# Kernel tuning notes

Measured on AMD Instinct MI355X. Metric: run time of the kernel, lower is better.

Reference implementation:

```python
import jax, jax.numpy as jnp
import numpy as np

N = 100000
E = 1600000
IN, HID, OUT = 128, 128, 64


def sage_conv(x, edge_index, W_l, W_r, b):
    # PyG SAGEConv with mean aggregation:
    # out = mean_{j in N(i)} x_j @ W_l + x_i @ W_r + b
    src, dst = edge_index[0], edge_index[1]
    msgs = x[src]                                            # [E, D] gather
    summed = jax.ops.segment_sum(msgs, dst, num_segments=N)  # [N, D] scatter-add
    deg = jax.ops.segment_sum(jnp.ones((E,), x.dtype), dst, num_segments=N)
    mean = summed / jnp.maximum(deg, 1.0)[:, None]
    return mean @ W_l + x @ W_r + b


def setup_inputs() -> dict:
    key = jax.random.key(0)
    ks = jax.random.split(key, 8)
    x = jax.random.normal(ks[0], (N, IN), dtype=jnp.float32)
    edge_index = jax.random.randint(ks[1], (2, E), 0, N, dtype=jnp.int64)
    s1 = 1.0 / np.sqrt(IN)
    s2 = 1.0 / np.sqrt(HID)
    W1_l = jax.random.uniform(ks[2], (IN, HID), jnp.float32, -s1, s1)
    W1_r = jax.random.uniform(ks[3], (IN, HID), jnp.float32, -s1, s1)
    b1 = jnp.zeros((HID,), jnp.float32)
    W2_l = jax.random.uniform(ks[4], (HID, OUT), jnp.float32, -s2, s2)
    W2_r = jax.random.uniform(ks[5], (HID, OUT), jnp.float32, -s2, s2)
    b2 = jnp.zeros((OUT,), jnp.float32)
    return {"x": x, "edge_index": edge_index, "W1_l": W1_l, "W1_r": W1_r,
            "b1": b1, "W2_l": W2_l, "W2_r": W2_r, "b2": b2}


def reference(x, edge_index, W1_l, W1_r, b1, W2_l, W2_r, b2):
    h = sage_conv(x, edge_index, W1_l, W1_r, b1)
    h = jax.nn.relu(h)
    out = sage_conv(h, edge_index, W2_l, W2_r, b2)
    return out
```

## Files before the change

### kernel.cpp

```cpp
#include <hip/hip_runtime.h>

#define NN 100000
#define NE 1600000
#define KB 782
#define BSH 7
#define MAXB 4096
#define PBLK 200

#define OFF_CC    0
#define OFF_RST   1024
#define OFF_RDG   101120
#define OFF_STAGE 201216
#define OFF_XB    3404288
#define OFF_XF8   9810432
#define OFF_MEANB 13013504
#define OFF_HB    19419648
#define OFF_W1LP  25825792
#define OFF_W1RP  (25825792 + 8192)
#define OFF_W2LP  (25825792 + 16384)
#define OFF_W2RP  (25825792 + 20480)

typedef __bf16 bf16x8 __attribute__((ext_vector_type(8)));
typedef float f32x4 __attribute__((ext_vector_type(4)));
typedef float f32x2 __attribute__((ext_vector_type(2)));

static __device__ __forceinline__ ushort f2bf(float f) {
    unsigned u = __float_as_uint(f);
    return (ushort)((u + 0x7fffu + ((u >> 16) & 1u)) >> 16);
}
static __device__ __forceinline__ float bflo(unsigned u) { return __uint_as_float(u << 16); }
static __device__ __forceinline__ float bfhi(unsigned u) { return __uint_as_float(u & 0xffff0000u); }

__global__ void cvt_kernel(const float* __restrict__ x, ushort* __restrict__ xb,
                           unsigned* __restrict__ xf8) {
    int i = blockIdx.x * 256 + threadIdx.x;
    float4 v = ((const float4*)x)[i];
    uint2 o;
    o.x = (unsigned)f2bf(v.x) | ((unsigned)f2bf(v.y) << 16);
    o.y = (unsigned)f2bf(v.z) | ((unsigned)f2bf(v.w) << 16);
    ((uint2*)xb)[i] = o;
    int p8 = __builtin_amdgcn_cvt_pk_fp8_f32(v.x, v.y, 0, false);
    p8 = __builtin_amdgcn_cvt_pk_fp8_f32(v.z, v.w, p8, true);
    xf8[i] = (unsigned)p8;
}

__global__ void pack_kernel(const float* __restrict__ W1l, const float* __restrict__ W1r,
                            const float* __restrict__ W2l, const float* __restrict__ W2r,
                            ushort* __restrict__ w1lp, ushort* __restrict__ w1rp,
                            ushort* __restrict__ w2lp, ushort* __restrict__ w2rp) {
    int blk = blockIdx.x;
    const float* W;
    ushort* out;
    int N, frag0;
    if (blk < 8)       { W = W1l; out = w1lp; N = 128; frag0 = blk * 4; }
    else if (blk < 16) { W = W1r; out = w1rp; N = 128; frag0 = (blk - 8) * 4; }
    else if (blk < 20) { W = W2l; out = w2lp; N = 64;  frag0 = (blk - 16) * 4; }
    else               { W = W2r; out = w2rp; N = 64;  frag0 = (blk - 20) * 4; }
    int lane = threadIdx.x & 63;
    int frag = frag0 + (threadIdx.x >> 6);
    int NT = N >> 4;
    int ktile = frag / NT, ntile = frag - ktile * NT;
    int k = ktile * 32 + (lane >> 4) * 8;
    int n = ntile * 16 + (lane & 15);
    ushort tmp[8];
#pragma unroll
    for (int j = 0; j < 8; ++j) tmp[j] = f2bf(W[(k + j) * N + n]);
    uint4 o;
    o.x = (unsigned)tmp[0] | ((unsigned)tmp[1] << 16);
    o.y = (unsigned)tmp[2] | ((unsigned)tmp[3] << 16);
    o.z = (unsigned)tmp[4] | ((unsigned)tmp[5] << 16);
    o.w = (unsigned)tmp[6] | ((unsigned)tmp[7] << 16);
    *(uint4*)&out[(frag * 64 + lane) * 8] = o;
}

__global__ __launch_bounds__(1024) void cpart_kernel(const int* __restrict__ src,
                                                     const int* __restrict__ dst,
                                                     int* __restrict__ cc,
                                                     unsigned* __restrict__ stage) {
    __shared__ int hist[KB];
    __shared__ int cur[KB];
    int t = threadIdx.x;
    int e0 = blockIdx.x * (NE / PBLK);
    int e1 = e0 + (NE / PBLK);
    for (int i = t; i < KB; i += 1024) hist[i] = 0;
    __syncthreads();
    for (int e = e0 + t; e < e1; e += 1024)
        atomicAdd(&hist[dst[e] >> BSH], 1);
    __syncthreads();
    for (int i = t; i < KB; i += 1024) {
        int c = hist[i];
        cur[i] = c ? atomicAdd(&cc[i], c) : 0;
    }
    __syncthreads();
    for (int e = e0 + t; e < e1; e += 1024) {
        int d = dst[e];
        int bkt = d >> BSH;
        int p = atomicAdd(&cur[bkt], 1);
        if (p < MAXB)
            stage[bkt * MAXB + p] = ((unsigned)(d & 127) << 17) | (unsigned)src[e];
    }
}

__global__ __launch_bounds__(256) void sort_kernel(unsigned* __restrict__ stage,
                                                   const int* __restrict__ cc,
                                                   int* __restrict__ rstart,
                                                   int* __restrict__ rdeg) {
    __shared__ unsigned ssrc[MAXB];
    __shared__ int sc[128];
    __shared__ int loff[129];
    __shared__ int lcur[128];
    int t = threadIdx.x;
    int b = blockIdx.x;
    unsigned* st = stage + b * MAXB;
    int cnt = min(cc[b], MAXB);

    if (t < 128) lcur[t] = 0;
    __syncthreads();
    for (int i = t; i < cnt; i += 256) atomicAdd(&lcur[st[i] >> 17], 1);
    __syncthreads();
    if (t < 128) sc[t] = lcur[t];
    __syncthreads();
    for (int off = 1; off < 128; off <<= 1) {
        int v = (t < 128 && t >= off) ? sc[t - off] : 0;
        __syncthreads();
        if (t < 128) sc[t] += v;
        __syncthreads();
    }
    if (t < 128) {
        int excl = (t == 0) ? 0 : sc[t - 1];
        loff[t] = excl;
        lcur[t] = excl;
    }
    if (t == 127) loff[128] = sc[127];
    __syncthreads();
    for (int i = t; i < cnt; i += 256) {
        unsigned v = st[i];
        int p = atomicAdd(&lcur[v >> 17], 1);
        ssrc[p] = v & 0x1FFFFu;
    }
    __syncthreads();
    for (int i = t; i < cnt; i += 256) st[i] = ssrc[i];
    int node0 = b << BSH;
    if (t < 128 && node0 + t < NN) {
        rstart[node0 + t] = b * MAXB + loff[t];
        rdeg[node0 + t] = loff[t + 1] - loff[t];
    }
}

static __device__ __forceinline__ void accum8(float* a, uint2 u) {
    f32x2 p0 = __builtin_amdgcn_cvt_pk_f32_fp8(u.x, false);
    f32x2 p1 = __builtin_amdgcn_cvt_pk_f32_fp8(u.x, true);
    f32x2 p2 = __builtin_amdgcn_cvt_pk_f32_fp8(u.y, false);
    f32x2 p3 = __builtin_amdgcn_cvt_pk_f32_fp8(u.y, true);
    a[0] += p0.x; a[1] += p0.y; a[2] += p1.x; a[3] += p1.y;
    a[4] += p2.x; a[5] += p2.y; a[6] += p3.x; a[7] += p3.y;
}

static __device__ __forceinline__ void writeRow8(ushort* __restrict__ meanb, int node,
                                                 int l4, const float* a, int deg) {
    float inv = 1.0f / fmaxf((float)deg, 1.0f);
    uint4 o;
    o.x = (unsigned)f2bf(a[0] * inv) | ((unsigned)f2bf(a[1] * inv) << 16);
    o.y = (unsigned)f2bf(a[2] * inv) | ((unsigned)f2bf(a[3] * inv) << 16);
    o.z = (unsigned)f2bf(a[4] * inv) | ((unsigned)f2bf(a[5] * inv) << 16);
    o.w = (unsigned)f2bf(a[6] * inv) | ((unsigned)f2bf(a[7] * inv) << 16);
    *(uint4*)&meanb[node * 128 + 8 * l4] = o;
}

__global__ __launch_bounds__(256) void agg1g_kernel(const unsigned* __restrict__ es,
                                                    const int* __restrict__ rstart,
                                                    const int* __restrict__ rdeg,
                                                    const unsigned* __restrict__ xf8,
                                                    ushort* __restrict__ meanb) {
    int t = threadIdx.x;
    int l4 = t & 15;
    int nA = blockIdx.x * 32 + (t >> 4) * 2;
    int nB = nA + 1;
    int sA = rstart[nA], dA = rdeg[nA];
    int sB = rstart[nB], dB = rdeg[nB];
    const uint2* xv = (const uint2*)xf8;
    float aA[8] = {0.f, 0.f, 0.f, 0.f, 0.f, 0.f, 0.f, 0.f};
    float aB[8] = {0.f, 0.f, 0.f, 0.f, 0.f, 0.f, 0.f, 0.f};
    int eA = 0, eB = 0;
    while (eA + 4 <= dA && eB + 4 <= dB) {
        int qa0 = es[sA + eA + 0], qa1 = es[sA + eA + 1];
        int qa2 = es[sA + eA + 2], qa3 = es[sA + eA + 3];
        int qb0 = es[sB + eB + 0], qb1 = es[sB + eB + 1];
        int qb2 = es[sB + eB + 2], qb3 = es[sB + eB + 3];
        uint2 ua0 = xv[qa0 * 16 + l4], ua1 = xv[qa1 * 16 + l4];
        uint2 ua2 = xv[qa2 * 16 + l4], ua3 = xv[qa3 * 16 + l4];
        uint2 ub0 = xv[qb0 * 16 + l4], ub1 = xv[qb1 * 16 + l4];
        uint2 ub2 = xv[qb2 * 16 + l4], ub3 = xv[qb3 * 16 + l4];
        accum8(aA, ua0); accum8(aA, ua1); accum8(aA, ua2); accum8(aA, ua3);
        accum8(aB, ub0); accum8(aB, ub1); accum8(aB, ub2); accum8(aB, ub3);
        eA += 4; eB += 4;
    }
    for (; eA + 4 <= dA; eA += 4) {
        int q0 = es[sA + eA + 0], q1 = es[sA + eA + 1];
        int q2 = es[sA + eA + 2], q3 = es[sA + eA + 3];
        uint2 u0 = xv[q0 * 16 + l4], u1 = xv[q1 * 16 + l4];
        uint2 u2 = xv[q2 * 16 + l4], u3 = xv[q3 * 16 + l4];
        accum8(aA, u0); accum8(aA, u1); accum8(aA, u2); accum8(aA, u3);
    }
    for (; eA < dA; ++eA) accum8(aA, xv[es[sA + eA] * 16 + l4]);
    for (; eB + 4 <= dB; eB += 4) {
        int q0 = es[sB + eB + 0], q1 = es[sB + eB + 1];
        int q2 = es[sB + eB + 2], q3 = es[sB + eB + 3];
        uint2 u0 = xv[q0 * 16 + l4], u1 = xv[q1 * 16 + l4];
        uint2 u2 = xv[q2 * 16 + l4], u3 = xv[q3 * 16 + l4];
        accum8(aB, u0); accum8(aB, u1); accum8(aB, u2); accum8(aB, u3);
    }
    for (; eB < dB; ++eB) accum8(aB, xv[es[sB + eB] * 16 + l4]);

    writeRow8(meanb, nA, l4, aA, dA);
    writeRow8(meanb, nB, l4, aB, dB);
}

__global__ __launch_bounds__(256) void agg2g_kernel(const unsigned* __restrict__ es,
                                                    const int* __restrict__ rstart,
                                                    const int* __restrict__ rdeg,
                                                    const ushort* __restrict__ pb,
                                                    float* __restrict__ meanp) {
    int t = threadIdx.x;
    int l5 = t & 31;
    int nA = blockIdx.x * 16 + (t >> 5) * 2;
    int nB = nA + 1;
    int sA = rstart[nA], dA = rdeg[nA];
    int sB = rstart[nB], dB = rdeg[nB];
    const unsigned* pbu = (const unsigned*)pb;
    float a0 = 0.f, a1 = 0.f, b0 = 0.f, b1 = 0.f;
    int eA = 0, eB = 0;
    while (eA + 4 <= dA && eB + 4 <= dB) {
        int qa0 = es[sA + eA + 0], qa1 = es[sA + eA + 1];
        int qa2 = es[sA + eA + 2], qa3 = es[sA + eA + 3];
        int qb0 = es[sB + eB + 0], qb1 = es[sB + eB + 1];
        int qb2 = es[sB + eB + 2], qb3 = es[sB + eB + 3];
        unsigned ua0 = pbu[qa0 * 32 + l5], ua1 = pbu[qa1 * 32 + l5];
        unsigned ua2 = pbu[qa2 * 32 + l5], ua3 = pbu[qa3 * 32 + l5];
        unsigned ub0 = pbu[qb0 * 32 + l5], ub1 = pbu[qb1 * 32 + l5];
        unsigned ub2 = pbu[qb2 * 32 + l5], ub3 = pbu[qb3 * 32 + l5];
        a0 += bflo(ua0) + bflo(ua1) + bflo(ua2) + bflo(ua3);
        a1 += bfhi(ua0) + bfhi(ua1) + bfhi(ua2) + bfhi(ua3);
        b0 += bflo(ub0) + bflo(ub1) + bflo(ub2) + bflo(ub3);
        b1 += bfhi(ub0) + bfhi(ub1) + bfhi(ub2) + bfhi(ub3);
        eA += 4; eB += 4;
    }
    for (; eA + 4 <= dA; eA += 4) {
        int q0 = es[sA + eA + 0], q1 = es[sA + eA + 1];
        int q2 = es[sA + eA + 2], q3 = es[sA + eA + 3];
        unsigned u0 = pbu[q0 * 32 + l5], u1 = pbu[q1 * 32 + l5];
        unsigned u2 = pbu[q2 * 32 + l5], u3 = pbu[q3 * 32 + l5];
        a0 += bflo(u0) + bflo(u1) + bflo(u2) + bflo(u3);
        a1 += bfhi(u0) + bfhi(u1) + bfhi(u2) + bfhi(u3);
    }
    for (; eA < dA; ++eA) {
        unsigned u = pbu[es[sA + eA] * 32 + l5];
        a0 += bflo(u); a1 += bfhi(u);
    }
    for (; eB + 4 <= dB; eB += 4) {
        int q0 = es[sB + eB + 0], q1 = es[sB + eB + 1];
        int q2 = es[sB + eB + 2], q3 = es[sB + eB + 3];
        unsigned u0 = pbu[q0 * 32 + l5], u1 = pbu[q1 * 32 + l5];
        unsigned u2 = pbu[q2 * 32 + l5], u3 = pbu[q3 * 32 + l5];
        b0 += bflo(u0) + bflo(u1) + bflo(u2) + bflo(u3);
        b1 += bfhi(u0) + bfhi(u1) + bfhi(u2) + bfhi(u3);
    }
    for (; eB < dB; ++eB) {
        unsigned u = pbu[es[sB + eB] * 32 + l5];
        b0 += bflo(u); b1 += bfhi(u);
    }
    float invA = 1.0f / fmaxf((float)dA, 1.0f);
    float invB = 1.0f / fmaxf((float)dB, 1.0f);
    float2 oA = {a0 * invA, a1 * invA};
    float2 oB = {b0 * invB, b1 * invB};
    *(float2*)&meanp[(size_t)nA * 64 + 2 * l5] = oA;
    *(float2*)&meanp[(size_t)nB * 64 + 2 * l5] = oB;
}

__global__ __launch_bounds__(256) void gemm1_kernel(const ushort* __restrict__ meanb,
                                                    const ushort* __restrict__ xb,
                                                    const ushort* __restrict__ w1lp,
                                                    const ushort* __restrict__ w1rp,
                                                    const float* __restrict__ b1,
                                                    const ushort* __restrict__ w2lp,
                                                    ushort* __restrict__ hb,
                                                    ushort* __restrict__ pb) {
    __shared__ ushort As[64 * 136];
    int t = threadIdx.x;
    int node0 = blockIdx.x * 64;
    int w = t >> 6, l = t & 63;
    int lrow = w * 16 + (l & 15);
    int lkq = (l >> 4) * 8;
    int cq = l & 15, rq = (l >> 4) * 4;

    f32x4 acc[8];
#pragma unroll
    for (int i = 0; i < 8; ++i) acc[i] = (f32x4){0.f, 0.f, 0.f, 0.f};

    {
        const uint4* g = (const uint4*)(meanb + (size_t)node0 * 128);
#pragma unroll
        for (int i = 0; i < 4; ++i) {
            int chunk = t + 256 * i;
            *(uint4*)&As[(chunk >> 4) * 136 + (chunk & 15) * 8] = g[chunk];
        }
    }
    __syncthreads();
#pragma unroll
    for (int kt = 0; kt < 4; ++kt) {
        bf16x8 a = *(const bf16x8*)&As[lrow * 136 + kt * 32 + lkq];
        const bf16x8* bp = (const bf16x8*)w1lp + (kt * 8) * 64 + l;
#pragma unroll
        for (int nt = 0; nt < 8; ++nt)
            acc[nt] = __builtin_amdgcn_mfma_f32_16x16x32_bf16(a, bp[nt * 64], acc[nt], 0, 0, 0);
    }
    __syncthreads();

    {
        const uint4* g = (const uint4*)(xb + (size_t)node0 * 128);
#pragma unroll
        for (int i = 0; i < 4; ++i) {
            int chunk = t + 256 * i;
            *(uint4*)&As[(chunk >> 4) * 136 + (chunk & 15) * 8] = g[chunk];
        }
    }
    __syncthreads();
#pragma unroll
    for (int kt = 0; kt < 4; ++kt) {
        bf16x8 a = *(const bf16x8*)&As[lrow * 136 + kt * 32 + lkq];
        const bf16x8* bp = (const bf16x8*)w1rp + (kt * 8) * 64 + l;
#pragma unroll
        for (int nt = 0; nt < 8; ++nt)
            acc[nt] = __builtin_amdgcn_mfma_f32_16x16x32_bf16(a, bp[nt * 64], acc[nt], 0, 0, 0);
    }
    __syncthreads();

#pragma unroll
    for (int nt = 0; nt < 8; ++nt) {
        int n = nt * 16 + cq;
        float bias = b1[n];
#pragma unroll
        for (int r = 0; r < 4; ++r) {
            float hv = fmaxf(acc[nt][r] + bias, 0.0f);
            As[(w * 16 + rq + r) * 136 + n] = f2bf(hv);
        }
    }
    __syncthreads();

    {
        uint4* g = (uint4*)(hb + (size_t)node0 * 128);
#pragma unroll
        for (int i = 0; i < 4; ++i) {
            int chunk = t + 256 * i;
            if (node0 + (chunk >> 4) < NN)
                g[chunk] = *(const uint4*)&As[(chunk >> 4) * 136 + (chunk & 15) * 8];
        }
    }

    f32x4 acc2[4];
#pragma unroll
    for (int i = 0; i < 4; ++i) acc2[i] = (f32x4){0.f, 0.f, 0.f, 0.f};
#pragma unroll
    for (int kt = 0; kt < 4; ++kt) {
        bf16x8 a = *(const bf16x8*)&As[lrow * 136 + kt * 32 + lkq];
        const bf16x8* bp = (const bf16x8*)w2lp + (kt * 4) * 64 + l;
#pragma unroll
        for (int nt = 0; nt < 4; ++nt)
            acc2[nt] = __builtin_amdgcn_mfma_f32_16x16x32_bf16(a, bp[nt * 64], acc2[nt], 0, 0, 0);
    }
    __syncthreads();

#pragma unroll
    for (int nt = 0; nt < 4; ++nt)
#pragma unroll
        for (int r = 0; r < 4; ++r)
            As[(w * 16 + rq + r) * 136 + nt * 16 + cq] = f2bf(acc2[nt][r]);
    __syncthreads();
    {
        uint4* g = (uint4*)(pb + (size_t)node0 * 64);
#pragma unroll
        for (int i = 0; i < 2; ++i) {
            int chunk = t + 256 * i;
            if (node0 + (chunk >> 3) < NN)
                g[chunk] = *(const uint4*)&As[(chunk >> 3) * 136 + (chunk & 7) * 8];
        }
    }
}

__global__ __launch_bounds__(256) void gemm2_kernel(const float* __restrict__ meanp,
                                                    const ushort* __restrict__ hb,
                                                    const ushort* __restrict__ w2rp,
                                                    const float* __restrict__ b2,
                                                    float* __restrict__ out) {
    __shared__ ushort As[64 * 136];
    int t = threadIdx.x;
    int node0 = blockIdx.x * 64;
    int w = t >> 6, l = t & 63;
    int lrow = w * 16 + (l & 15);
    int lkq = (l >> 4) * 8;
    int cq = l & 15, rq = (l >> 4) * 4;

    {
        const uint4* g = (const uint4*)(hb + (size_t)node0 * 128);
#pragma unroll
        for (int i = 0; i < 4; ++i) {
            int chunk = t + 256 * i;
            *(uint4*)&As[(chunk >> 4) * 136 + (chunk & 15) * 8] = g[chunk];
        }
    }
    __syncthreads();

    f32x4 acc[4];
#pragma unroll
    for (int i = 0; i < 4; ++i) acc[i] = (f32x4){0.f, 0.f, 0.f, 0.f};
#pragma unroll
    for (int kt = 0; kt < 4; ++kt) {
        bf16x8 a = *(const bf16x8*)&As[lrow * 136 + kt * 32 + lkq];
        const bf16x8* bp = (const bf16x8*)w2rp + (kt * 4) * 64 + l;
#pragma unroll
        for (int nt = 0; nt < 4; ++nt)
            acc[nt] = __builtin_amdgcn_mfma_f32_16x16x32_bf16(a, bp[nt * 64], acc[nt], 0, 0, 0);
    }

#pragma unroll
    for (int nt = 0; nt < 4; ++nt) {
        int n = nt * 16 + cq;
        float bias = b2[n];
#pragma unroll
        for (int r = 0; r < 4; ++r) {
            int row = node0 + w * 16 + rq + r;
            if (row < NN)
                out[(size_t)row * 64 + n] = acc[nt][r] + bias + meanp[(size_t)row * 64 + n];
        }
    }
}

extern "C" void kernel_launch(void* const* d_in, const int* in_sizes, int n_in,
                              void* d_out, int out_size, void* d_ws, size_t ws_size,
                              hipStream_t stream) {
    const float* x   = (const float*)d_in[0];
    const int*   ei  = (const int*)d_in[1];
    const float* W1l = (const float*)d_in[2];
    const float* W1r = (const float*)d_in[3];
    const float* b1  = (const float*)d_in[4];
    const float* W2l = (const float*)d_in[5];
    const float* W2r = (const float*)d_in[6];
    const float* b2  = (const float*)d_in[7];

    const int* src = ei;
    const int* dst = ei + NE;

    int*      ws_i   = (int*)d_ws;
    int*      cc     = ws_i + OFF_CC;
    int*      rstart = ws_i + OFF_RST;
    int*      rdeg   = ws_i + OFF_RDG;
    unsigned* stage  = (unsigned*)(ws_i + OFF_STAGE);
    ushort*   xb     = (ushort*)(ws_i + OFF_XB);
    unsigned* xf8    = (unsigned*)(ws_i + OFF_XF8);
    ushort*   pb     = (ushort*)(ws_i + OFF_XF8);
    ushort*   meanb  = (ushort*)(ws_i + OFF_MEANB);
    float*    meanp  = (float*)(ws_i + OFF_MEANB);
    ushort*   hb     = (ushort*)(ws_i + OFF_HB);
    ushort*   w1lp   = (ushort*)(ws_i + OFF_W1LP);
    ushort*   w1rp   = (ushort*)(ws_i + OFF_W1RP);
    ushort*   w2lp   = (ushort*)(ws_i + OFF_W2LP);
    ushort*   w2rp   = (ushort*)(ws_i + OFF_W2RP);

    hipMemsetAsync(cc, 0, 1024 * sizeof(int), stream);
    cvt_kernel<<<12500, 256, 0, stream>>>(x, xb, xf8);
    pack_kernel<<<24, 256, 0, stream>>>(W1l, W1r, W2l, W2r, w1lp, w1rp, w2lp, w2rp);
    cpart_kernel<<<PBLK, 1024, 0, stream>>>(src, dst, cc, stage);
    sort_kernel<<<KB, 256, 0, stream>>>(stage, cc, rstart, rdeg);

    agg1g_kernel<<<NN / 32, 256, 0, stream>>>(stage, rstart, rdeg, xf8, meanb);
    gemm1_kernel<<<(NN + 63) / 64, 256, 0, stream>>>(meanb, xb, w1lp, w1rp, b1, w2lp, hb, pb);

    agg2g_kernel<<<NN / 16, 256, 0, stream>>>(stage, rstart, rdeg, pb, meanp);
    gemm2_kernel<<<(NN + 63) / 64, 256, 0, stream>>>(meanp, hb, w2rp, b2, (float*)d_out);
}
```

Measured before the change: 268.9 us.

## Fuse prep kernels and fold layer-2 root GEMM into layer-1 GEMM

Merges the conversion, weight-packing and edge-partition kernels into a single prep launch, running the partition part with 256-thread blocks instead of 1024. Layer-1's GEMM now also computes h@W2_r+b2 and writes it straight to the output, so the separate gemm2 kernel and the hb buffer round-trip go away. The layer-2 aggregation then read-modify-writes the output, adding the mean term in place. This removes two launches and an intermediate buffer, at the cost of extra registers in gemm1 and a read of the output in agg2.

```diff
diff --git a/kernel.cpp b/kernel.cpp
--- a/kernel.cpp
+++ b/kernel.cpp
@@ -14,7 +14,6 @@
 #define OFF_XB    3404288
 #define OFF_XF8   9810432
 #define OFF_MEANB 13013504
-#define OFF_HB    19419648
 #define OFF_W1LP  25825792
 #define OFF_W1RP  (25825792 + 8192)
 #define OFF_W2LP  (25825792 + 16384)
@@ -31,68 +30,76 @@
 static __device__ __forceinline__ float bflo(unsigned u) { return __uint_as_float(u << 16); }
 static __device__ __forceinline__ float bfhi(unsigned u) { return __uint_as_float(u & 0xffff0000u); }
 
-__global__ void cvt_kernel(const float* __restrict__ x, ushort* __restrict__ xb,
-                           unsigned* __restrict__ xf8) {
-    int i = blockIdx.x * 256 + threadIdx.x;
-    float4 v = ((const float4*)x)[i];
-    uint2 o;
-    o.x = (unsigned)f2bf(v.x) | ((unsigned)f2bf(v.y) << 16);
-    o.y = (unsigned)f2bf(v.z) | ((unsigned)f2bf(v.w) << 16);
-    ((uint2*)xb)[i] = o;
-    int p8 = __builtin_amdgcn_cvt_pk_fp8_f32(v.x, v.y, 0, false);
-    p8 = __builtin_amdgcn_cvt_pk_fp8_f32(v.z, v.w, p8, true);
-    xf8[i] = (unsigned)p8;
-}
-
-__global__ void pack_kernel(const float* __restrict__ W1l, const float* __restrict__ W1r,
-                            const float* __restrict__ W2l, const float* __restrict__ W2r,
-                            ushort* __restrict__ w1lp, ushort* __restrict__ w1rp,
-                            ushort* __restrict__ w2lp, ushort* __restrict__ w2rp) {
-    int blk = blockIdx.x;
-    const float* W;
-    ushort* out;
-    int N, frag0;
-    if (blk < 8)       { W = W1l; out = w1lp; N = 128; frag0 = blk * 4; }
-    else if (blk < 16) { W = W1r; out = w1rp; N = 128; frag0 = (blk - 8) * 4; }
-    else if (blk < 20) { W = W2l; out = w2lp; N = 64;  frag0 = (blk - 16) * 4; }
-    else               { W = W2r; out = w2rp; N = 64;  frag0 = (blk - 20) * 4; }
-    int lane = threadIdx.x & 63;
-    int frag = frag0 + (threadIdx.x >> 6);
-    int NT = N >> 4;
-    int ktile = frag / NT, ntile = frag - ktile * NT;
-    int k = ktile * 32 + (lane >> 4) * 8;
-    int n = ntile * 16 + (lane & 15);
-    ushort tmp[8];
-#pragma unroll
-    for (int j = 0; j < 8; ++j) tmp[j] = f2bf(W[(k + j) * N + n]);
-    uint4 o;
-    o.x = (unsigned)tmp[0] | ((unsigned)tmp[1] << 16);
-    o.y = (unsigned)tmp[2] | ((unsigned)tmp[3] << 16);
-    o.z = (unsigned)tmp[4] | ((unsigned)tmp[5] << 16);
-    o.w = (unsigned)tmp[6] | ((unsigned)tmp[7] << 16);
-    *(uint4*)&out[(frag * 64 + lane) * 8] = o;
-}
-
-__global__ __launch_bounds__(1024) void cpart_kernel(const int* __restrict__ src,
-                                                     const int* __restrict__ dst,
-                                                     int* __restrict__ cc,
-                                                     unsigned* __restrict__ stage) {
+#define PREP_CPART 200
+#define PREP_PACK  24
+#define PREP_CVT   12500
+
+__global__ __launch_bounds__(256) void prep_kernel(
+    const float* __restrict__ x, ushort* __restrict__ xb, unsigned* __restrict__ xf8,
+    const float* __restrict__ W1l, const float* __restrict__ W1r,
+    const float* __restrict__ W2l, const float* __restrict__ W2r,
+    ushort* __restrict__ w1lp, ushort* __restrict__ w1rp,
+    ushort* __restrict__ w2lp, ushort* __restrict__ w2rp,
+    const int* __restrict__ src, const int* __restrict__ dst,
+    int* __restrict__ cc, unsigned* __restrict__ stage) {
     __shared__ int hist[KB];
     __shared__ int cur[KB];
+    int bid = blockIdx.x;
     int t = threadIdx.x;
-    int e0 = blockIdx.x * (NE / PBLK);
+
+    if (bid >= PREP_CPART + PREP_PACK) {
+        int i = (bid - PREP_CPART - PREP_PACK) * 256 + t;
+        float4 v = ((const float4*)x)[i];
+        uint2 o;
+        o.x = (unsigned)f2bf(v.x) | ((unsigned)f2bf(v.y) << 16);
+        o.y = (unsigned)f2bf(v.z) | ((unsigned)f2bf(v.w) << 16);
+        ((uint2*)xb)[i] = o;
+        int p8 = __builtin_amdgcn_cvt_pk_fp8_f32(v.x, v.y, 0, false);
+        p8 = __builtin_amdgcn_cvt_pk_fp8_f32(v.z, v.w, p8, true);
+        xf8[i] = (unsigned)p8;
+        return;
+    }
+
+    if (bid >= PREP_CPART) {
+        int blk = bid - PREP_CPART;
+        const float* W;
+        ushort* out;
+        int N, frag0;
+        if (blk < 8)       { W = W1l; out = w1lp; N = 128; frag0 = blk * 4; }
+        else if (blk < 16) { W = W1r; out = w1rp; N = 128; frag0 = (blk - 8) * 4; }
+        else if (blk < 20) { W = W2l; out = w2lp; N = 64;  frag0 = (blk - 16) * 4; }
+        else               { W = W2r; out = w2rp; N = 64;  frag0 = (blk - 20) * 4; }
+        int lane = t & 63;
+        int frag = frag0 + (t >> 6);
+        int NT = N >> 4;
+        int ktile = frag / NT, ntile = frag - ktile * NT;
+        int k = ktile * 32 + (lane >> 4) * 8;
+        int n = ntile * 16 + (lane & 15);
+        ushort tmp[8];
+#pragma unroll
+        for (int j = 0; j < 8; ++j) tmp[j] = f2bf(W[(k + j) * N + n]);
+        uint4 o;
+        o.x = (unsigned)tmp[0] | ((unsigned)tmp[1] << 16);
+        o.y = (unsigned)tmp[2] | ((unsigned)tmp[3] << 16);
+        o.z = (unsigned)tmp[4] | ((unsigned)tmp[5] << 16);
+        o.w = (unsigned)tmp[6] | ((unsigned)tmp[7] << 16);
+        *(uint4*)&out[(frag * 64 + lane) * 8] = o;
+        return;
+    }
+
+    int e0 = bid * (NE / PBLK);
     int e1 = e0 + (NE / PBLK);
-    for (int i = t; i < KB; i += 1024) hist[i] = 0;
-    __syncthreads();
-    for (int e = e0 + t; e < e1; e += 1024)
+    for (int i = t; i < KB; i += 256) hist[i] = 0;
+    __syncthreads();
+    for (int e = e0 + t; e < e1; e += 256)
         atomicAdd(&hist[dst[e] >> BSH], 1);
     __syncthreads();
-    for (int i = t; i < KB; i += 1024) {
+    for (int i = t; i < KB; i += 256) {
         int c = hist[i];
         cur[i] = c ? atomicAdd(&cc[i], c) : 0;
     }
     __syncthreads();
-    for (int e = e0 + t; e < e1; e += 1024) {
+    for (int e = e0 + t; e < e1; e += 256) {
         int d = dst[e];
         int bkt = d >> BSH;
         int p = atomicAdd(&cur[bkt], 1);
@@ -220,13 +227,15 @@
                                                     const int* __restrict__ rstart,
                                                     const int* __restrict__ rdeg,
                                                     const ushort* __restrict__ pb,
-                                                    float* __restrict__ meanp) {
+                                                    float* __restrict__ out) {
     int t = threadIdx.x;
     int l5 = t & 31;
     int nA = blockIdx.x * 16 + (t >> 5) * 2;
     int nB = nA + 1;
     int sA = rstart[nA], dA = rdeg[nA];
     int sB = rstart[nB], dB = rdeg[nB];
+    float2 pA = *(const float2*)&out[(size_t)nA * 64 + 2 * l5];
+    float2 pB = *(const float2*)&out[(size_t)nB * 64 + 2 * l5];
     const unsigned* pbu = (const unsigned*)pb;
     float a0 = 0.f, a1 = 0.f, b0 = 0.f, b1 = 0.f;
     int eA = 0, eB = 0;
@@ -271,10 +280,10 @@
     }
     float invA = 1.0f / fmaxf((float)dA, 1.0f);
     float invB = 1.0f / fmaxf((float)dB, 1.0f);
-    float2 oA = {a0 * invA, a1 * invA};
-    float2 oB = {b0 * invB, b1 * invB};
-    *(float2*)&meanp[(size_t)nA * 64 + 2 * l5] = oA;
-    *(float2*)&meanp[(size_t)nB * 64 + 2 * l5] = oB;
+    float2 oA = {pA.x + a0 * invA, pA.y + a1 * invA};
+    float2 oB = {pB.x + b0 * invB, pB.y + b1 * invB};
+    *(float2*)&out[(size_t)nA * 64 + 2 * l5] = oA;
+    *(float2*)&out[(size_t)nB * 64 + 2 * l5] = oB;
 }
 
 __global__ __launch_bounds__(256) void gemm1_kernel(const ushort* __restrict__ meanb,
@@ -283,114 +292,9 @@
                                                     const ushort* __restrict__ w1rp,
                                                     const float* __restrict__ b1,
                                                     const ushort* __restrict__ w2lp,
-                                                    ushort* __restrict__ hb,
-                                                    ushort* __restrict__ pb) {
-    __shared__ ushort As[64 * 136];
-    int t = threadIdx.x;
-    int node0 = blockIdx.x * 64;
-    int w = t >> 6, l = t & 63;
-    int lrow = w * 16 + (l & 15);
-    int lkq = (l >> 4) * 8;
-    int cq = l & 15, rq = (l >> 4) * 4;
-
-    f32x4 acc[8];
-#pragma unroll
-    for (int i = 0; i < 8; ++i) acc[i] = (f32x4){0.f, 0.f, 0.f, 0.f};
-
-    {
-        const uint4* g = (const uint4*)(meanb + (size_t)node0 * 128);
-#pragma unroll
-        for (int i = 0; i < 4; ++i) {
-            int chunk = t + 256 * i;
-            *(uint4*)&As[(chunk >> 4) * 136 + (chunk & 15) * 8] = g[chunk];
-        }
-    }
-    __syncthreads();
-#pragma unroll
-    for (int kt = 0; kt < 4; ++kt) {
-        bf16x8 a = *(const bf16x8*)&As[lrow * 136 + kt * 32 + lkq];
-        const bf16x8* bp = (const bf16x8*)w1lp + (kt * 8) * 64 + l;
-#pragma unroll
-        for (int nt = 0; nt < 8; ++nt)
-            acc[nt] = __builtin_amdgcn_mfma_f32_16x16x32_bf16(a, bp[nt * 64], acc[nt], 0, 0, 0);
-    }
-    __syncthreads();
-
-    {
-        const uint4* g = (const uint4*)(xb + (size_t)node0 * 128);
-#pragma unroll
-        for (int i = 0; i < 4; ++i) {
-            int chunk = t + 256 * i;
-            *(uint4*)&As[(chunk >> 4) * 136 + (chunk & 15) * 8] = g[chunk];
-        }
-    }
-    __syncthreads();
-#pragma unroll
-    for (int kt = 0; kt < 4; ++kt) {
-        bf16x8 a = *(const bf16x8*)&As[lrow * 136 + kt * 32 + lkq];
-        const bf16x8* bp = (const bf16x8*)w1rp + (kt * 8) * 64 + l;
-#pragma unroll
-        for (int nt = 0; nt < 8; ++nt)
-            acc[nt] = __builtin_amdgcn_mfma_f32_16x16x32_bf16(a, bp[nt * 64], acc[nt], 0, 0, 0);
-    }
-    __syncthreads();
-
-#pragma unroll
-    for (int nt = 0; nt < 8; ++nt) {
-        int n = nt * 16 + cq;
-        float bias = b1[n];
-#pragma unroll
-        for (int r = 0; r < 4; ++r) {
-            float hv = fmaxf(acc[nt][r] + bias, 0.0f);
-            As[(w * 16 + rq + r) * 136 + n] = f2bf(hv);
-        }
-    }
-    __syncthreads();
-
-    {
-        uint4* g = (uint4*)(hb + (size_t)node0 * 128);
-#pragma unroll
-        for (int i = 0; i < 4; ++i) {
-            int chunk = t + 256 * i;
-            if (node0 + (chunk >> 4) < NN)
-                g[chunk] = *(const uint4*)&As[(chunk >> 4) * 136 + (chunk & 15) * 8];
-        }
-    }
-
-    f32x4 acc2[4];
-#pragma unroll
-    for (int i = 0; i < 4; ++i) acc2[i] = (f32x4){0.f, 0.f, 0.f, 0.f};
-#pragma unroll
-    for (int kt = 0; kt < 4; ++kt) {
-        bf16x8 a = *(const bf16x8*)&As[lrow * 136 + kt * 32 + lkq];
-        const bf16x8* bp = (const bf16x8*)w2lp + (kt * 4) * 64 + l;
-#pragma unroll
-        for (int nt = 0; nt < 4; ++nt)
-            acc2[nt] = __builtin_amdgcn_mfma_f32_16x16x32_bf16(a, bp[nt * 64], acc2[nt], 0, 0, 0);
-    }
-    __syncthreads();
-
-#pragma unroll
-    for (int nt = 0; nt < 4; ++nt)
-#pragma unroll
-        for (int r = 0; r < 4; ++r)
-            As[(w * 16 + rq + r) * 136 + nt * 16 + cq] = f2bf(acc2[nt][r]);
-    __syncthreads();
-    {
-        uint4* g = (uint4*)(pb + (size_t)node0 * 64);
-#pragma unroll
-        for (int i = 0; i < 2; ++i) {
-            int chunk = t + 256 * i;
-            if (node0 + (chunk >> 3) < NN)
-                g[chunk] = *(const uint4*)&As[(chunk >> 3) * 136 + (chunk & 7) * 8];
-        }
-    }
-}
-
-__global__ __launch_bounds__(256) void gemm2_kernel(const float* __restrict__ meanp,
-                                                    const ushort* __restrict__ hb,
                                                     const ushort* __restrict__ w2rp,
                                                     const float* __restrict__ b2,
+                                                    ushort* __restrict__ pb,
                                                     float* __restrict__ out) {
     __shared__ ushort As[64 * 136];
     int t = threadIdx.x;
@@ -400,8 +304,12 @@
     int lkq = (l >> 4) * 8;
     int cq = l & 15, rq = (l >> 4) * 4;
 
+    f32x4 acc[8];
+#pragma unroll
+    for (int i = 0; i < 8; ++i) acc[i] = (f32x4){0.f, 0.f, 0.f, 0.f};
+
     {
-        const uint4* g = (const uint4*)(hb + (size_t)node0 * 128);
+        const uint4* g = (const uint4*)(meanb + (size_t)node0 * 128);
 #pragma unroll
         for (int i = 0; i < 4; ++i) {
             int chunk = t + 256 * i;
@@ -409,17 +317,64 @@
         }
     }
     __syncthreads();
-
-    f32x4 acc[4];
-#pragma unroll
-    for (int i = 0; i < 4; ++i) acc[i] = (f32x4){0.f, 0.f, 0.f, 0.f};
 #pragma unroll
     for (int kt = 0; kt < 4; ++kt) {
         bf16x8 a = *(const bf16x8*)&As[lrow * 136 + kt * 32 + lkq];
-        const bf16x8* bp = (const bf16x8*)w2rp + (kt * 4) * 64 + l;
-#pragma unroll
-        for (int nt = 0; nt < 4; ++nt)
+        const bf16x8* bp = (const bf16x8*)w1lp + (kt * 8) * 64 + l;
+#pragma unroll
+        for (int nt = 0; nt < 8; ++nt)
             acc[nt] = __builtin_amdgcn_mfma_f32_16x16x32_bf16(a, bp[nt * 64], acc[nt], 0, 0, 0);
+    }
+    __syncthreads();
+
+    {
+        const uint4* g = (const uint4*)(xb + (size_t)node0 * 128);
+#pragma unroll
+        for (int i = 0; i < 4; ++i) {
+            int chunk = t + 256 * i;
+            *(uint4*)&As[(chunk >> 4) * 136 + (chunk & 15) * 8] = g[chunk];
+        }
+    }
+    __syncthreads();
+#pragma unroll
+    for (int kt = 0; kt < 4; ++kt) {
+        bf16x8 a = *(const bf16x8*)&As[lrow * 136 + kt * 32 + lkq];
+        const bf16x8* bp = (const bf16x8*)w1rp + (kt * 8) * 64 + l;
+#pragma unroll
+        for (int nt = 0; nt < 8; ++nt)
+            acc[nt] = __builtin_amdgcn_mfma_f32_16x16x32_bf16(a, bp[nt * 64], acc[nt], 0, 0, 0);
+    }
+    __syncthreads();
+
+#pragma unroll
+    for (int nt = 0; nt < 8; ++nt) {
+        int n = nt * 16 + cq;
+        float bias = b1[n];
+#pragma unroll
+        for (int r = 0; r < 4; ++r) {
+            float hv = fmaxf(acc[nt][r] + bias, 0.0f);
+            As[(w * 16 + rq + r) * 136 + n] = f2bf(hv);
+        }
+    }
+    __syncthreads();
+
+    f32x4 acc2[4];
+    f32x4 acc3[4];
+#pragma unroll
+    for (int i = 0; i < 4; ++i) {
+        acc2[i] = (f32x4){0.f, 0.f, 0.f, 0.f};
+        acc3[i] = (f32x4){0.f, 0.f, 0.f, 0.f};
+    }
+#pragma unroll
+    for (int kt = 0; kt < 4; ++kt) {
+        bf16x8 a = *(const bf16x8*)&As[lrow * 136 + kt * 32 + lkq];
+        const bf16x8* bpl = (const bf16x8*)w2lp + (kt * 4) * 64 + l;
+        const bf16x8* bpr = (const bf16x8*)w2rp + (kt * 4) * 64 + l;
+#pragma unroll
+        for (int nt = 0; nt < 4; ++nt) {
+            acc2[nt] = __builtin_amdgcn_mfma_f32_16x16x32_bf16(a, bpl[nt * 64], acc2[nt], 0, 0, 0);
+            acc3[nt] = __builtin_amdgcn_mfma_f32_16x16x32_bf16(a, bpr[nt * 64], acc3[nt], 0, 0, 0);
+        }
     }
 
 #pragma unroll
@@ -430,7 +385,24 @@
         for (int r = 0; r < 4; ++r) {
             int row = node0 + w * 16 + rq + r;
             if (row < NN)
-                out[(size_t)row * 64 + n] = acc[nt][r] + bias + meanp[(size_t)row * 64 + n];
+                out[(size_t)row * 64 + n] = acc3[nt][r] + bias;
+        }
+    }
+
+    __syncthreads();
+#pragma unroll
+    for (int nt = 0; nt < 4; ++nt)
+#pragma unroll
+        for (int r = 0; r < 4; ++r)
+            As[(w * 16 + rq + r) * 136 + nt * 16 + cq] = f2bf(acc2[nt][r]);
+    __syncthreads();
+    {
+        uint4* g = (uint4*)(pb + (size_t)node0 * 64);
+#pragma unroll
+        for (int i = 0; i < 2; ++i) {
+            int chunk = t + 256 * i;
+            if (node0 + (chunk >> 3) < NN)
+                g[chunk] = *(const uint4*)&As[(chunk >> 3) * 136 + (chunk & 7) * 8];
         }
     }
 }
@@ -459,22 +431,20 @@
     unsigned* xf8    = (unsigned*)(ws_i + OFF_XF8);
     ushort*   pb     = (ushort*)(ws_i + OFF_XF8);
     ushort*   meanb  = (ushort*)(ws_i + OFF_MEANB);
-    float*    meanp  = (float*)(ws_i + OFF_MEANB);
-    ushort*   hb     = (ushort*)(ws_i + OFF_HB);
     ushort*   w1lp   = (ushort*)(ws_i + OFF_W1LP);
     ushort*   w1rp   = (ushort*)(ws_i + OFF_W1RP);
     ushort*   w2lp   = (ushort*)(ws_i + OFF_W2LP);
     ushort*   w2rp   = (ushort*)(ws_i + OFF_W2RP);
 
     hipMemsetAsync(cc, 0, 1024 * sizeof(int), stream);
-    cvt_kernel<<<12500, 256, 0, stream>>>(x, xb, xf8);
-    pack_kernel<<<24, 256, 0, stream>>>(W1l, W1r, W2l, W2r, w1lp, w1rp, w2lp, w2rp);
-    cpart_kernel<<<PBLK, 1024, 0, stream>>>(src, dst, cc, stage);
+
+    prep_kernel<<<PREP_CPART + PREP_PACK + PREP_CVT, 256, 0, stream>>>(
+        x, xb, xf8, W1l, W1r, W2l, W2r, w1lp, w1rp, w2lp, w2rp, src, dst, cc, stage);
     sort_kernel<<<KB, 256, 0, stream>>>(stage, cc, rstart, rdeg);
 
     agg1g_kernel<<<NN / 32, 256, 0, stream>>>(stage, rstart, rdeg, xf8, meanb);
-    gemm1_kernel<<<(NN + 63) / 64, 256, 0, stream>>>(meanb, xb, w1lp, w1rp, b1, w2lp, hb, pb);
-
-    agg2g_kernel<<<NN / 16, 256, 0, stream>>>(stage, rstart, rdeg, pb, meanp);
-    gemm2_kernel<<<(NN + 63) / 64, 256, 0, stream>>>(meanp, hb, w2rp, b2, (float*)d_out);
-}
+    gemm1_kernel<<<(NN + 63) / 64, 256, 0, stream>>>(meanb, xb, w1lp, w1rp, b1,
+                                                     w2lp, w2rp, b2, pb, (float*)d_out);
+
+    agg2g_kernel<<<NN / 16, 256, 0, stream>>>(stage, rstart, rdeg, pb, (float*)d_out);
+}
```

After: 268.8 us. Within noise of the previous version (-0.0%).
